# Kernel tuning notes

Measured on AMD Instinct MI355X. Metric: run time of the kernel, lower is better.

Reference implementation:

```python
import jax, jax.numpy as jnp
import numpy as np

B, S, D, H = 2, 2048, 1024, 16
DK = D // H


def layernorm(x, gamma, bias, eps=1e-6):
    m = jnp.mean(x, axis=-1, keepdims=True)
    v = jnp.mean((x - m) ** 2, axis=-1, keepdims=True)  # biased var (correction=0)
    return gamma * (x - m) / jnp.sqrt(v + eps) + bias


def setup_inputs() -> dict:
    key = jax.random.key(0)
    ks = jax.random.split(key, 10)
    xav = (2.0 / (D + D)) ** 0.5  # xavier_normal_ std for square [D,D]
    lin1_b = (1.0 / D) ** 0.5     # nn.Linear default init bound
    lin2_b = (1.0 / (4 * D)) ** 0.5
    return {
        "X": jax.random.normal(ks[0], (B, S, D), jnp.float32),
        "padding_mask": jnp.ones((B, 1, S), jnp.int32),
        "W_Q": jax.random.normal(ks[1], (D, D), jnp.float32) * xav,
        "W_K": jax.random.normal(ks[2], (D, D), jnp.float32) * xav,
        "W_V": jax.random.normal(ks[3], (D, D), jnp.float32) * xav,
        "W_O": jax.random.normal(ks[4], (D, D), jnp.float32) * xav,
        "g1": jnp.ones((D,), jnp.float32),
        "b1": jnp.zeros((D,), jnp.float32),
        "W1": jax.random.uniform(ks[5], (D, 4 * D), jnp.float32, -lin1_b, lin1_b),
        "bias1": jax.random.uniform(ks[6], (4 * D,), jnp.float32, -lin1_b, lin1_b),
        "W2": jax.random.uniform(ks[7], (4 * D, D), jnp.float32, -lin2_b, lin2_b),
        "bias2": jax.random.uniform(ks[8], (D,), jnp.float32, -lin2_b, lin2_b),
        "g2": jnp.ones((D,), jnp.float32),
        "b2": jnp.zeros((D,), jnp.float32),
    }


def reference(X, padding_mask, W_Q, W_K, W_V, W_O, g1, b1, W1, bias1, W2, bias2, g2, b2):
    b, s, d = X.shape
    # pre-norm + MHA
    xn = layernorm(X, g1, b1)
    q = (xn @ W_Q).reshape(b, s, H, DK).transpose(0, 2, 1, 3)  # [B,H,S,DK]
    k = (xn @ W_K).reshape(b, s, H, DK).transpose(0, 2, 1, 3)
    v = (xn @ W_V).reshape(b, s, H, DK).transpose(0, 2, 1, 3)
    scores = jnp.einsum("bhqd,bhkd->bhqk", q, k) / np.sqrt(DK).astype(np.float32)
    mask = padding_mask[:, None, :, :]  # [B,1,1,S] broadcast over heads/queries
    scores = jnp.where(mask == 0, jnp.float32(-1e9), scores)
    w = jax.nn.softmax(scores, axis=-1)
    attn = jnp.einsum("bhqk,bhkd->bhqd", w, v)
    attn = attn.transpose(0, 2, 1, 3).reshape(b, s, d) @ W_O
    out = attn + X
    # pre-norm + GELU FFN (exact erf GELU, matching nn.GELU default)
    nn2 = layernorm(out, g2, b2)
    ff = jax.nn.gelu(nn2 @ W1 + bias1, approximate=False) @ W2 + bias2
    return ff + out
```

## Files before the change

kernel.cpp:

```cpp
#include <hip/hip_runtime.h>
#include <hip/hip_bf16.h>


using bf16 = __hip_bfloat16;
typedef __attribute__((ext_vector_type(4))) float f32x4;
typedef __attribute__((ext_vector_type(16))) float f32x16;
typedef __attribute__((ext_vector_type(8))) short bf16x8;

#define DEVI static __device__ __forceinline__

DEVI void async_copy16(const void* g, void* l) {
  __builtin_amdgcn_global_load_lds(
      (const __attribute__((address_space(1))) void*)g,
      (__attribute__((address_space(3))) void*)l, 16, 0, 0);
}

DEVI ushort f2bf_bits(float v) {
  __hip_bfloat16 h = __float2bfloat16(v);
  return *reinterpret_cast<ushort*>(&h);
}

DEVI float bfbits2f(ushort u) {
  union { float f; unsigned int i; } x;
  x.i = ((unsigned int)u) << 16;
  return x.f;
}

DEVI unsigned int pk2(float lo, float hi) {
  return (unsigned int)f2bf_bits(lo) | ((unsigned int)f2bf_bits(hi) << 16);
}

__global__ __launch_bounds__(256) void ln_kernel(
    const float* __restrict__ in, const float* __restrict__ gamma,
    const float* __restrict__ beta, bf16* __restrict__ out) {
  const long row = blockIdx.x;
  const int t = threadIdx.x;
  float4 x = ((const float4*)(in + row * 1024))[t];
  float s = x.x + x.y + x.z + x.w;
  float s2 = x.x * x.x + x.y * x.y + x.z * x.z + x.w * x.w;
#pragma unroll
  for (int m = 1; m < 64; m <<= 1) {
    s += __shfl_xor(s, m);
    s2 += __shfl_xor(s2, m);
  }
  __shared__ float red[8];
  const int w = t >> 6, l = t & 63;
  if (l == 0) { red[w] = s; red[4 + w] = s2; }
  __syncthreads();
  s = red[0] + red[1] + red[2] + red[3];
  s2 = red[4] + red[5] + red[6] + red[7];
  const float mean = s * (1.0f / 1024.0f);
  const float var = s2 * (1.0f / 1024.0f) - mean * mean;
  const float rstd = rsqrtf(var + 1e-6f);
  float4 g4 = ((const float4*)gamma)[t];
  float4 b4 = ((const float4*)beta)[t];
  union { ushort h[4]; uint2 u; } o;
  o.h[0] = f2bf_bits(g4.x * (x.x - mean) * rstd + b4.x);
  o.h[1] = f2bf_bits(g4.y * (x.y - mean) * rstd + b4.y);
  o.h[2] = f2bf_bits(g4.z * (x.z - mean) * rstd + b4.z);
  o.h[3] = f2bf_bits(g4.w * (x.w - mean) * rstd + b4.w);
  ((uint2*)(out + row * 1024))[t] = o.u;
}

__global__ __launch_bounds__(256) void oproj_reduce_ln(
    const float* __restrict__ p0, const float* __restrict__ p1,
    const float* __restrict__ X, const float* __restrict__ gamma,
    const float* __restrict__ beta, float* __restrict__ res_out,
    bf16* __restrict__ xn_out) {
  const long row = blockIdx.x;
  const int t = threadIdx.x;
  const long i = row * 256 + t;
  const float4 a = ((const float4*)p0)[i];
  const float4 b = ((const float4*)p1)[i];
  const float4 c = ((const float4*)X)[i];
  float4 x;
  x.x = a.x + b.x + c.x; x.y = a.y + b.y + c.y;
  x.z = a.z + b.z + c.z; x.w = a.w + b.w + c.w;
  ((float4*)res_out)[i] = x;
  float s = x.x + x.y + x.z + x.w;
  float s2 = x.x * x.x + x.y * x.y + x.z * x.z + x.w * x.w;
#pragma unroll
  for (int m = 1; m < 64; m <<= 1) {
    s += __shfl_xor(s, m);
    s2 += __shfl_xor(s2, m);
  }
  __shared__ float red[8];
  const int w = t >> 6, l = t & 63;
  if (l == 0) { red[w] = s; red[4 + w] = s2; }
  __syncthreads();
  s = red[0] + red[1] + red[2] + red[3];
  s2 = red[4] + red[5] + red[6] + red[7];
  const float mean = s * (1.0f / 1024.0f);
  const float var = s2 * (1.0f / 1024.0f) - mean * mean;
  const float rstd = rsqrtf(var + 1e-6f);
  float4 g4 = ((const float4*)gamma)[t];
  float4 b4 = ((const float4*)beta)[t];
  union { ushort h[4]; uint2 u; } o;
  o.h[0] = f2bf_bits(g4.x * (x.x - mean) * rstd + b4.x);
  o.h[1] = f2bf_bits(g4.y * (x.y - mean) * rstd + b4.y);
  o.h[2] = f2bf_bits(g4.z * (x.z - mean) * rstd + b4.z);
  o.h[3] = f2bf_bits(g4.w * (x.w - mean) * rstd + b4.w);
  ((uint2*)(xn_out + row * 1024))[t] = o.u;
}

__global__ __launch_bounds__(256) void transpose_all(
    const float* __restrict__ q, const float* __restrict__ k,
    const float* __restrict__ v, const float* __restrict__ o,
    const float* __restrict__ w1, const float* __restrict__ w2,
    bf16* __restrict__ wqkvo, bf16* __restrict__ w1t, bf16* __restrict__ w2t) {
  const int tid = blockIdx.x;
  const float* W;
  bf16* Wt;
  int K, N, n0, k0;
  if (tid < 4096) {
    const int z = tid >> 10, r = tid & 1023;
    W = (z == 0) ? q : (z == 1) ? k : (z == 2) ? v : o;
    Wt = wqkvo + (size_t)z * 1024 * 1024;
    K = 1024; N = 1024; n0 = (r & 31) << 5; k0 = (r >> 5) << 5;
  } else if (tid < 8192) {
    const int r = tid - 4096;
    W = w1; Wt = w1t; K = 1024; N = 4096;
    n0 = (r & 127) << 5; k0 = (r >> 7) << 5;
  } else {
    const int r = tid - 8192;
    W = w2; Wt = w2t; K = 4096; N = 1024;
    n0 = (r & 31) << 5; k0 = (r >> 5) << 5;
  }
  __shared__ float tile[32][33];
  const int tx = threadIdx.x & 31, ty = threadIdx.x >> 5;
#pragma unroll
  for (int i = 0; i < 32; i += 8)
    tile[ty + i][tx] = W[(long)(k0 + ty + i) * N + n0 + tx];
  __syncthreads();
#pragma unroll
  for (int i = 0; i < 32; i += 8)
    Wt[(long)(n0 + ty + i) * K + k0 + tx] = __float2bfloat16(tile[tx][ty + i]);
}

template <int EPI, int KSPLIT>
__global__ __launch_bounds__(256) void gemm_bt(
    const bf16* __restrict__ A, const bf16* __restrict__ Bt,
    const int M, const int N, const int K, const int lda, const int ldb,
    const float* __restrict__ bias, const float* __restrict__ res,
    float* __restrict__ pother, void* __restrict__ Cout) {
  __shared__ __align__(16) char gsmem[65536];
  const int t = threadIdx.x;
  const int w = t >> 6, l = t & 63;
  const int nb = N >> 7;
  const int cpx = gridDim.x >> 3;
  int bidx = (blockIdx.x & 7) * cpx + (blockIdx.x >> 3);
  int sl = 0;
  if (KSPLIT == 2) {
    const int half = gridDim.x >> 1;
    sl = bidx >= half;
    bidx -= sl * half;
  }
  const int bm = bidx / nb, bn = bidx % nb;
  const long row0 = (long)bm << 7, col0 = (long)bn << 7;
  const int wr = (w >> 1) << 6, wc = (w & 1) << 6;
  const int lr = l & 15;
  const int lkb = (l >> 4) << 4;

  f32x4 acc[4][4];
#pragma unroll
  for (int m = 0; m < 4; ++m)
#pragma unroll
    for (int n = 0; n < 4; ++n) acc[m][n] = (f32x4){0.f, 0.f, 0.f, 0.f};

  const int rA = t >> 3;
  const int g = (t & 7) ^ ((t >> 3) & 7);
  const bf16* gA = A + (row0 + rA) * (long)lda + (long)sl * K + g * 8;
  const bf16* gB = Bt + (col0 + rA) * (long)ldb + (long)sl * K + g * 8;

  const int nt = K >> 6;
#pragma unroll
  for (int cr = 0; cr < 4; ++cr) {
    async_copy16(gA + (long)cr * 32 * lda, gsmem + t * 16 + cr * 4096);
    async_copy16(gB + (long)cr * 32 * ldb, gsmem + 16384 + t * 16 + cr * 4096);
  }
  int cur = 0;

  for (int kt = 0; kt < nt; ++kt) {
    if (kt < nt - 1) {
      const int k1 = (kt + 1) << 6;
      char* dst = gsmem + (cur ^ 1) * 32768;
#pragma unroll
      for (int cr = 0; cr < 4; ++cr) {
        async_copy16(gA + (long)cr * 32 * lda + k1, dst + t * 16 + cr * 4096);
        async_copy16(gB + (long)cr * 32 * ldb + k1, dst + 16384 + t * 16 + cr * 4096);
      }
      asm volatile("s_waitcnt vmcnt(8)" ::: "memory");
    } else {
      asm volatile("s_waitcnt vmcnt(0)" ::: "memory");
    }
    __builtin_amdgcn_s_barrier();
    __builtin_amdgcn_sched_barrier(0);
    const char* As = gsmem + cur * 32768;
    const char* Bs = As + 16384;
#pragma unroll
    for (int ks = 0; ks < 2; ++ks) {
      bf16x8 af[4], bfr[4];
#pragma unroll
      for (int m = 0; m < 4; ++m) {
        const int row = wr + m * 16 + lr;
        af[m] = *(const bf16x8*)(As +
            (row * 128 + ((ks * 64 + lkb) ^ ((row & 7) << 4))));
      }
#pragma unroll
      for (int n = 0; n < 4; ++n) {
        const int row = wc + n * 16 + lr;
        bfr[n] = *(const bf16x8*)(Bs +
            (row * 128 + ((ks * 64 + lkb) ^ ((row & 7) << 4))));
      }
#pragma unroll
      for (int m = 0; m < 4; ++m)
#pragma unroll
        for (int n = 0; n < 4; ++n)
          acc[m][n] = __builtin_amdgcn_mfma_f32_16x16x32_bf16(af[m], bfr[n], acc[m][n], 0, 0, 0);
    }
    __builtin_amdgcn_sched_barrier(0);
    __builtin_amdgcn_s_barrier();
    cur ^= 1;
  }

  bf16* Cb = (bf16*)Cout;
  float* Cf = (float*)Cout;
  if ((EPI == 4 || EPI == 5) && sl == 1) Cf = pother;
#pragma unroll
  for (int m = 0; m < 4; ++m) {
#pragma unroll
    for (int r = 0; r < 4; ++r) {
      const long crow = row0 + wr + m * 16 + ((l >> 4) << 2) + r;
      const long rbase = crow * N;
#pragma unroll
      for (int n = 0; n < 4; ++n) {
        const long ccol = col0 + wc + n * 16 + lr;
        float v = acc[m][n][r];
        if (EPI == 2) {
          const float vv = v + bias[ccol];
          const float u2 = vv * (1.5957691216f + 0.0713548162f * vv * vv);
          v = vv / (1.0f + __expf(-u2));
        }
        if (EPI == 5 && sl == 0) v += bias[ccol] + res[rbase + ccol];
        if (EPI == 0 || EPI == 2)
          Cb[rbase + ccol] = __float2bfloat16(v);
        else
          Cf[rbase + ccol] = v;
      }
    }
  }
}

__global__ __launch_bounds__(256) void ff2_reduce(
    const float* __restrict__ p0, const float* __restrict__ p1,
    float* __restrict__ out) {
  const int idx = blockIdx.x * 256 + threadIdx.x;
  const float4 x = ((const float4*)p0)[idx];
  const float4 y = ((const float4*)p1)[idx];
  float4 a;
  a.x = x.x + y.x; a.y = x.y + y.y; a.z = x.z + y.z; a.w = x.w + y.w;
  ((float4*)out)[idx] = a;
}

__global__ __launch_bounds__(512) void attn_kernel(
    const bf16* __restrict__ QKV, const int* __restrict__ pmask,
    bf16* __restrict__ Oout) {
  const int bh = blockIdx.x;
  const int b = bh >> 4, h = bh & 15;
  const int q0 = blockIdx.y << 8;
  const int t = threadIdx.x;
  const int w = t >> 6, l = t & 63;
  const int lq = l & 31, hi = l >> 5;

  __shared__ __align__(16) char smem[65536];

  const long base = (long)b * 2048 * 3072;
  const bf16* Qg = QKV + base + h * 64;
  const bf16* Kg = QKV + base + 1024 + h * 64;
  const bf16* Vg = QKV + base + 2048 + h * 64;

  int kSrc[2], kDst[2], vk[2], vsg[2];
#pragma unroll
  for (int p = 0; p < 2; ++p) {
    const int c = p * 512 + t;
    const int kr = c >> 3;
    kSrc[p] = kr * 3072 + (((c & 7) ^ (kr & 7)) << 3);
    kDst[p] = c * 16;
    vk[p] = c >> 3;
    vsg[p] = c & 7;
  }

  const int qw0 = q0 + w * 32;
  bf16x8 qf[4];
#pragma unroll
  for (int dc = 0; dc < 4; ++dc) {
    uint4 raw = *(const uint4*)(Qg + (long)(qw0 + lq) * 3072 + dc * 16 + hi * 8);
    union { uint4 u4; ushort us[8]; } in; in.u4 = raw;
    union { bf16x8 v; ushort us[8]; } o;
#pragma unroll
    for (int e = 0; e < 8; ++e) o.us[e] = f2bf_bits(0.125f * bfbits2f(in.us[e]));
    qf[dc] = o.v;
  }

  union { unsigned int u[4]; bf16x8 v; } bones;
  bones.u[0] = (hi == 0) ? 0x00003F80u : 0u;
  bones.u[1] = bones.u[2] = bones.u[3] = 0u;

  uint4 vreg[2];
#pragma unroll
  for (int p = 0; p < 2; ++p) {
    vreg[p] = *(const uint4*)(Vg + (long)vk[p] * 3072 + vsg[p] * 8);
    async_copy16(Kg + kSrc[p], smem + kDst[p]);
  }
#pragma unroll
  for (int p = 0; p < 2; ++p) {
    const ushort* vs = (const ushort*)&vreg[p];
#pragma unroll
    for (int e = 0; e < 8; ++e) {
      const int d = vsg[p] * 8 + e;
      *(ushort*)(smem + 32768 + d * 256 +
                 ((vk[p] * 2) ^ (((e ^ vsg[p]) & 7) << 4))) = vs[e];
    }
  }

  f32x16 oacc[2];
#pragma unroll
  for (int nt = 0; nt < 2; ++nt)
#pragma unroll
    for (int r = 0; r < 16; ++r) oacc[nt][r] = 0.f;
  float mrun = -3.0e38f, lsum = 0.f;
  int cur = 0;

  __syncthreads();

  for (int ktg = 0; ktg < 16; ++ktg) {
    if (ktg < 15) {
      const long nrow0 = (long)(ktg + 1) * 128 * 3072;
#pragma unroll
      for (int p = 0; p < 2; ++p) {
        vreg[p] = *(const uint4*)(Vg + nrow0 + (long)vk[p] * 3072 + vsg[p] * 8);
        async_copy16(Kg + nrow0 + kSrc[p], smem + (cur ^ 1) * 16384 + kDst[p]);
      }
    }
    const int k0 = ktg << 7;
    const char* Ks = smem + cur * 16384;
    const char* Vt = smem + 32768 + cur * 16384;

    f32x16 sacc[4];
    __builtin_amdgcn_s_setprio(1);
#pragma unroll
    for (int kt = 0; kt < 4; ++kt) {
#pragma unroll
      for (int r = 0; r < 16; ++r) sacc[kt][r] = 0.f;
#pragma unroll
      for (int dc = 0; dc < 4; ++dc) {
        bf16x8 ka = *(const bf16x8*)(Ks +
            ((kt * 32 + lq) * 128 + ((dc * 32 + hi * 16) ^ ((lq & 7) << 4))));
        sacc[kt] = __builtin_amdgcn_mfma_f32_32x32x16_bf16(ka, qf[dc], sacc[kt], 0, 0, 0);
      }
      const int mv = pmask[b * 2048 + k0 + kt * 32 + lq];
      union { unsigned int u[4]; bf16x8 v; } aadd;
      aadd.u[0] = (hi == 0 && mv == 0) ? (unsigned int)f2bf_bits(-1.0e9f) : 0u;
      aadd.u[1] = aadd.u[2] = aadd.u[3] = 0u;
      sacc[kt] = __builtin_amdgcn_mfma_f32_32x32x16_bf16(aadd.v, bones.v, sacc[kt], 0, 0, 0);
    }
    __builtin_amdgcn_s_setprio(0);

    float tmax = -3.0e38f;
#pragma unroll
    for (int kt = 0; kt < 4; ++kt)
#pragma unroll
      for (int r = 0; r < 16; ++r) tmax = fmaxf(tmax, sacc[kt][r]);
    tmax = fmaxf(tmax, __shfl_xor(tmax, 32));
    const bool need = (bool)__any(tmax > mrun + 8.0f);
    const float mnew = need ? fmaxf(mrun, tmax) : mrun;
    float psum = 0.f;
#pragma unroll
    for (int kt = 0; kt < 4; ++kt)
#pragma unroll
      for (int r = 0; r < 16; ++r) {
        const float p = __expf(sacc[kt][r] - mnew);
        sacc[kt][r] = p;
        psum += p;
      }
    psum += __shfl_xor(psum, 32);
    if (need) {
      const float alpha = __expf(mrun - mnew);
      mrun = mnew;
      lsum = lsum * alpha + psum;
#pragma unroll
      for (int r = 0; r < 16; ++r) {
        const float ar = __shfl(alpha, (r & 3) + 8 * (r >> 2) + 4 * hi);
        oacc[0][r] *= ar;
        oacc[1][r] *= ar;
      }
    } else {
      lsum += psum;
    }

    union { unsigned int u[4]; bf16x8 v; } paE[4], paO[4];
#pragma unroll
    for (int kt = 0; kt < 4; ++kt) {
      const unsigned int cs0 = pk2(sacc[kt][0], sacc[kt][1]);
      const unsigned int cs1 = pk2(sacc[kt][2], sacc[kt][3]);
      const unsigned int cs2 = pk2(sacc[kt][4], sacc[kt][5]);
      const unsigned int cs3 = pk2(sacc[kt][6], sacc[kt][7]);
      const unsigned int cs4 = pk2(sacc[kt][8], sacc[kt][9]);
      const unsigned int cs5 = pk2(sacc[kt][10], sacc[kt][11]);
      const unsigned int cs6 = pk2(sacc[kt][12], sacc[kt][13]);
      const unsigned int cs7 = pk2(sacc[kt][14], sacc[kt][15]);
      const unsigned int es0 = __shfl_xor(cs0, 32);
      const unsigned int es1 = __shfl_xor(cs1, 32);
      const unsigned int es2 = __shfl_xor(cs2, 32);
      const unsigned int es3 = __shfl_xor(cs3, 32);
      const unsigned int es4 = __shfl_xor(cs4, 32);
      const unsigned int es5 = __shfl_xor(cs5, 32);
      const unsigned int es6 = __shfl_xor(cs6, 32);
      const unsigned int es7 = __shfl_xor(cs7, 32);
      paE[kt].u[0] = hi ? es2 : cs0;
      paE[kt].u[1] = hi ? es3 : cs1;
      paE[kt].u[2] = hi ? cs2 : es0;
      paE[kt].u[3] = hi ? cs3 : es1;
      paO[kt].u[0] = hi ? es6 : cs4;
      paO[kt].u[1] = hi ? es7 : cs5;
      paO[kt].u[2] = hi ? cs6 : es4;
      paO[kt].u[3] = hi ? cs7 : es5;
    }

    __builtin_amdgcn_s_setprio(1);
#pragma unroll
    for (int kt = 0; kt < 4; ++kt)
#pragma unroll
      for (int nt = 0; nt < 2; ++nt) {
        const int vrow = nt * 32 + lq;
        const int vsw = ((vrow & 7) ^ ((vrow >> 3) & 7)) << 4;
        bf16x8 vbE = *(const bf16x8*)(Vt + (vrow * 256 + ((kt * 64 + hi * 16) ^ vsw)));
        oacc[nt] = __builtin_amdgcn_mfma_f32_32x32x16_bf16(paE[kt].v, vbE, oacc[nt], 0, 0, 0);
        bf16x8 vbO = *(const bf16x8*)(Vt + (vrow * 256 + ((kt * 64 + 32 + hi * 16) ^ vsw)));
        oacc[nt] = __builtin_amdgcn_mfma_f32_32x32x16_bf16(paO[kt].v, vbO, oacc[nt], 0, 0, 0);
      }
    __builtin_amdgcn_s_setprio(0);

    if (ktg < 15) {
      char* VtN = smem + 32768 + (cur ^ 1) * 16384;
#pragma unroll
      for (int p = 0; p < 2; ++p) {
        const ushort* vs = (const ushort*)&vreg[p];
#pragma unroll
        for (int e = 0; e < 8; ++e) {
          const int d = vsg[p] * 8 + e;
          *(ushort*)(VtN + d * 256 +
                     ((vk[p] * 2) ^ (((e ^ vsg[p]) & 7) << 4))) = vs[e];
        }
      }
    }

    __syncthreads();
    cur ^= 1;
  }

  const float inv = 1.0f / lsum;
#pragma unroll
  for (int r = 0; r < 16; ++r) {
    const int crow = (r & 3) + 8 * (r >> 2) + 4 * hi;
    const float ir = __shfl(inv, crow);
    const long orow = (long)b * 2048 + qw0 + crow;
#pragma unroll
    for (int nt = 0; nt < 2; ++nt)
      Oout[orow * 1024 + h * 64 + nt * 32 + lq] = __float2bfloat16(oacc[nt][r] * ir);
  }
}

extern "C" void kernel_launch(void* const* d_in, const int* in_sizes, int n_in,
                              void* d_out, int out_size, void* d_ws, size_t ws_size,
                              hipStream_t stream) {
  const float* X = (const float*)d_in[0];
  const int* pmask = (const int*)d_in[1];
  const float* W_Q = (const float*)d_in[2];
  const float* W_K = (const float*)d_in[3];
  const float* W_V = (const float*)d_in[4];
  const float* W_O = (const float*)d_in[5];
  const float* g1 = (const float*)d_in[6];
  const float* b1 = (const float*)d_in[7];
  const float* W1 = (const float*)d_in[8];
  const float* bias1 = (const float*)d_in[9];
  const float* W2 = (const float*)d_in[10];
  const float* bias2 = (const float*)d_in[11];
  const float* g2 = (const float*)d_in[12];
  const float* b2 = (const float*)d_in[13];
  (void)in_sizes; (void)n_in; (void)out_size; (void)ws_size;

  char* ws = (char*)d_ws;
  const size_t MB = 1ull << 20;
  bf16* W1_t   = (bf16*)(ws + 0);
  bf16* Wqkv_t = (bf16*)(ws + 8 * MB);
  bf16* Wo_t   = (bf16*)(ws + 14 * MB);
  bf16* W2_t   = (bf16*)(ws + 16 * MB);
  bf16* xn     = (bf16*)(ws + 24 * MB);
  bf16* QKV    = (bf16*)(ws + 32 * MB);
  bf16* attnb  = (bf16*)(ws + 56 * MB);
  bf16* ff1    = (bf16*)(ws + 32 * MB);
  float* p0o   = (float*)(ws + 64 * MB);
  float* p1o   = (float*)(ws + 32 * MB);
  float* p0    = (float*)(ws + 64 * MB);
  float* p1    = (float*)(ws + 0);
  float* res1  = (float*)d_out;

  transpose_all<<<12288, 256, 0, stream>>>(W_Q, W_K, W_V, W_O, W1, W2,
                                           Wqkv_t, W1_t, W2_t);
  ln_kernel<<<4096, 256, 0, stream>>>(X, g1, b1, xn);
  gemm_bt<0, 1><<<32 * 24, 256, 0, stream>>>(xn, Wqkv_t, 4096, 3072, 1024, 1024, 1024,
                                             nullptr, nullptr, nullptr, QKV);
  attn_kernel<<<dim3(32, 8), 512, 0, stream>>>(QKV, pmask, attnb);
  gemm_bt<4, 2><<<2 * 32 * 8, 256, 0, stream>>>(attnb, Wo_t, 4096, 1024, 512, 1024, 1024,
                                                nullptr, nullptr, p1o, p0o);
  oproj_reduce_ln<<<4096, 256, 0, stream>>>(p0o, p1o, X, g2, b2, res1, xn);
  gemm_bt<2, 1><<<32 * 32, 256, 0, stream>>>(xn, W1_t, 4096, 4096, 1024, 1024, 1024,
                                             bias1, nullptr, nullptr, ff1);
  gemm_bt<5, 2><<<2 * 32 * 8, 256, 0, stream>>>(ff1, W2_t, 4096, 1024, 2048, 4096, 4096,
                                                bias2, res1, p1, p0);
  ff2_reduce<<<4096, 256, 0, stream>>>(p0, p1, res1);
}
```

Baseline: 267.6 us.

## Triple-buffer GEMM A tiles with deeper prefetch and fuse LN1 into transpose

The GEMM now keeps three LDS buffers for the A tile and two for B. A is prefetched two k-steps ahead and B one step ahead, with the vmcnt waits adjusted to match. This is meant to hide more global-load latency in the main loop, but raises LDS use from 64KB to 80KB per block, which may cut occupancy. Separately, the first layernorm is folded into the weight-transpose kernel as extra blocks, removing one kernel launch.

```diff
diff --git a/kernel.cpp b/kernel.cpp
--- a/kernel.cpp
+++ b/kernel.cpp
@@ -30,36 +30,70 @@
   return (unsigned int)f2bf_bits(lo) | ((unsigned int)f2bf_bits(hi) << 16);
 }
 
-__global__ __launch_bounds__(256) void ln_kernel(
-    const float* __restrict__ in, const float* __restrict__ gamma,
-    const float* __restrict__ beta, bf16* __restrict__ out) {
-  const long row = blockIdx.x;
-  const int t = threadIdx.x;
-  float4 x = ((const float4*)(in + row * 1024))[t];
-  float s = x.x + x.y + x.z + x.w;
-  float s2 = x.x * x.x + x.y * x.y + x.z * x.z + x.w * x.w;
-#pragma unroll
-  for (int m = 1; m < 64; m <<= 1) {
-    s += __shfl_xor(s, m);
-    s2 += __shfl_xor(s2, m);
-  }
-  __shared__ float red[8];
-  const int w = t >> 6, l = t & 63;
-  if (l == 0) { red[w] = s; red[4 + w] = s2; }
+__global__ __launch_bounds__(256) void transpose_all_ln(
+    const float* __restrict__ q, const float* __restrict__ k,
+    const float* __restrict__ v, const float* __restrict__ o,
+    const float* __restrict__ w1, const float* __restrict__ w2,
+    bf16* __restrict__ wqkvo, bf16* __restrict__ w1t, bf16* __restrict__ w2t,
+    const float* __restrict__ X, const float* __restrict__ g1,
+    const float* __restrict__ b1, bf16* __restrict__ xn) {
+  const int tid = blockIdx.x;
+  if (tid >= 12288) {
+    const long row = tid - 12288;
+    const int t = threadIdx.x;
+    float4 x = ((const float4*)(X + row * 1024))[t];
+    float s = x.x + x.y + x.z + x.w;
+    float s2 = x.x * x.x + x.y * x.y + x.z * x.z + x.w * x.w;
+#pragma unroll
+    for (int m = 1; m < 64; m <<= 1) {
+      s += __shfl_xor(s, m);
+      s2 += __shfl_xor(s2, m);
+    }
+    __shared__ float red[8];
+    const int w = t >> 6, l = t & 63;
+    if (l == 0) { red[w] = s; red[4 + w] = s2; }
+    __syncthreads();
+    s = red[0] + red[1] + red[2] + red[3];
+    s2 = red[4] + red[5] + red[6] + red[7];
+    const float mean = s * (1.0f / 1024.0f);
+    const float var = s2 * (1.0f / 1024.0f) - mean * mean;
+    const float rstd = rsqrtf(var + 1e-6f);
+    float4 g4 = ((const float4*)g1)[t];
+    float4 b4 = ((const float4*)b1)[t];
+    union { ushort h[4]; uint2 u; } oo;
+    oo.h[0] = f2bf_bits(g4.x * (x.x - mean) * rstd + b4.x);
+    oo.h[1] = f2bf_bits(g4.y * (x.y - mean) * rstd + b4.y);
+    oo.h[2] = f2bf_bits(g4.z * (x.z - mean) * rstd + b4.z);
+    oo.h[3] = f2bf_bits(g4.w * (x.w - mean) * rstd + b4.w);
+    ((uint2*)(xn + row * 1024))[t] = oo.u;
+    return;
+  }
+  const float* W;
+  bf16* Wt;
+  int K, N, n0, k0;
+  if (tid < 4096) {
+    const int z = tid >> 10, r = tid & 1023;
+    W = (z == 0) ? q : (z == 1) ? k : (z == 2) ? v : o;
+    Wt = wqkvo + (size_t)z * 1024 * 1024;
+    K = 1024; N = 1024; n0 = (r & 31) << 5; k0 = (r >> 5) << 5;
+  } else if (tid < 8192) {
+    const int r = tid - 4096;
+    W = w1; Wt = w1t; K = 1024; N = 4096;
+    n0 = (r & 127) << 5; k0 = (r >> 7) << 5;
+  } else {
+    const int r = tid - 8192;
+    W = w2; Wt = w2t; K = 4096; N = 1024;
+    n0 = (r & 31) << 5; k0 = (r >> 5) << 5;
+  }
+  __shared__ float tile[32][33];
+  const int tx = threadIdx.x & 31, ty = threadIdx.x >> 5;
+#pragma unroll
+  for (int i = 0; i < 32; i += 8)
+    tile[ty + i][tx] = W[(long)(k0 + ty + i) * N + n0 + tx];
   __syncthreads();
-  s = red[0] + red[1] + red[2] + red[3];
-  s2 = red[4] + red[5] + red[6] + red[7];
-  const float mean = s * (1.0f / 1024.0f);
-  const float var = s2 * (1.0f / 1024.0f) - mean * mean;
-  const float rstd = rsqrtf(var + 1e-6f);
-  float4 g4 = ((const float4*)gamma)[t];
-  float4 b4 = ((const float4*)beta)[t];
-  union { ushort h[4]; uint2 u; } o;
-  o.h[0] = f2bf_bits(g4.x * (x.x - mean) * rstd + b4.x);
-  o.h[1] = f2bf_bits(g4.y * (x.y - mean) * rstd + b4.y);
-  o.h[2] = f2bf_bits(g4.z * (x.z - mean) * rstd + b4.z);
-  o.h[3] = f2bf_bits(g4.w * (x.w - mean) * rstd + b4.w);
-  ((uint2*)(out + row * 1024))[t] = o.u;
+#pragma unroll
+  for (int i = 0; i < 32; i += 8)
+    Wt[(long)(n0 + ty + i) * K + k0 + tx] = __float2bfloat16(tile[tx][ty + i]);
 }
 
 __global__ __launch_bounds__(256) void oproj_reduce_ln(
@@ -103,47 +137,13 @@
   ((uint2*)(xn_out + row * 1024))[t] = o.u;
 }
 
-__global__ __launch_bounds__(256) void transpose_all(
-    const float* __restrict__ q, const float* __restrict__ k,
-    const float* __restrict__ v, const float* __restrict__ o,
-    const float* __restrict__ w1, const float* __restrict__ w2,
-    bf16* __restrict__ wqkvo, bf16* __restrict__ w1t, bf16* __restrict__ w2t) {
-  const int tid = blockIdx.x;
-  const float* W;
-  bf16* Wt;
-  int K, N, n0, k0;
-  if (tid < 4096) {
-    const int z = tid >> 10, r = tid & 1023;
-    W = (z == 0) ? q : (z == 1) ? k : (z == 2) ? v : o;
-    Wt = wqkvo + (size_t)z * 1024 * 1024;
-    K = 1024; N = 1024; n0 = (r & 31) << 5; k0 = (r >> 5) << 5;
-  } else if (tid < 8192) {
-    const int r = tid - 4096;
-    W = w1; Wt = w1t; K = 1024; N = 4096;
-    n0 = (r & 127) << 5; k0 = (r >> 7) << 5;
-  } else {
-    const int r = tid - 8192;
-    W = w2; Wt = w2t; K = 4096; N = 1024;
-    n0 = (r & 31) << 5; k0 = (r >> 5) << 5;
-  }
-  __shared__ float tile[32][33];
-  const int tx = threadIdx.x & 31, ty = threadIdx.x >> 5;
-#pragma unroll
-  for (int i = 0; i < 32; i += 8)
-    tile[ty + i][tx] = W[(long)(k0 + ty + i) * N + n0 + tx];
-  __syncthreads();
-#pragma unroll
-  for (int i = 0; i < 32; i += 8)
-    Wt[(long)(n0 + ty + i) * K + k0 + tx] = __float2bfloat16(tile[tx][ty + i]);
-}
-
 template <int EPI, int KSPLIT>
 __global__ __launch_bounds__(256) void gemm_bt(
     const bf16* __restrict__ A, const bf16* __restrict__ Bt,
     const int M, const int N, const int K, const int lda, const int ldb,
     const float* __restrict__ bias, const float* __restrict__ res,
     float* __restrict__ pother, void* __restrict__ Cout) {
-  __shared__ __align__(16) char gsmem[65536];
+  __shared__ __align__(16) char gsmem[81920];
   const int t = threadIdx.x;
   const int w = t >> 6, l = t & 63;
   const int nb = N >> 7;
@@ -171,32 +171,46 @@
   const int g = (t & 7) ^ ((t >> 3) & 7);
   const bf16* gA = A + (row0 + rA) * (long)lda + (long)sl * K + g * 8;
   const bf16* gB = Bt + (col0 + rA) * (long)ldb + (long)sl * K + g * 8;
+  char* const Bbase = gsmem + 49152;
 
   const int nt = K >> 6;
 #pragma unroll
-  for (int cr = 0; cr < 4; ++cr) {
+  for (int cr = 0; cr < 4; ++cr)
     async_copy16(gA + (long)cr * 32 * lda, gsmem + t * 16 + cr * 4096);
-    async_copy16(gB + (long)cr * 32 * ldb, gsmem + 16384 + t * 16 + cr * 4096);
-  }
-  int cur = 0;
+#pragma unroll
+  for (int cr = 0; cr < 4; ++cr)
+    async_copy16(gB + (long)cr * 32 * ldb, Bbase + t * 16 + cr * 4096);
+#pragma unroll
+  for (int cr = 0; cr < 4; ++cr)
+    async_copy16(gA + (long)cr * 32 * lda + 64, gsmem + 16384 + t * 16 + cr * 4096);
+  int curB = 0;
 
   for (int kt = 0; kt < nt; ++kt) {
-    if (kt < nt - 1) {
+    if (kt + 1 < nt) {
       const int k1 = (kt + 1) << 6;
-      char* dst = gsmem + (cur ^ 1) * 32768;
-#pragma unroll
-      for (int cr = 0; cr < 4; ++cr) {
-        async_copy16(gA + (long)cr * 32 * lda + k1, dst + t * 16 + cr * 4096);
-        async_copy16(gB + (long)cr * 32 * ldb + k1, dst + 16384 + t * 16 + cr * 4096);
-      }
+      char* dstB = Bbase + (curB ^ 1) * 16384;
+#pragma unroll
+      for (int cr = 0; cr < 4; ++cr)
+        async_copy16(gB + (long)cr * 32 * ldb + k1, dstB + t * 16 + cr * 4096);
+    }
+    if (kt + 2 < nt) {
+      const int k2 = (kt + 2) << 6;
+      char* dstA = gsmem + ((kt + 2) % 3) * 16384;
+#pragma unroll
+      for (int cr = 0; cr < 4; ++cr)
+        async_copy16(gA + (long)cr * 32 * lda + k2, dstA + t * 16 + cr * 4096);
+    }
+    if (kt < nt - 2) {
+      asm volatile("s_waitcnt vmcnt(12)" ::: "memory");
+    } else if (kt == nt - 2) {
       asm volatile("s_waitcnt vmcnt(8)" ::: "memory");
     } else {
       asm volatile("s_waitcnt vmcnt(0)" ::: "memory");
     }
     __builtin_amdgcn_s_barrier();
     __builtin_amdgcn_sched_barrier(0);
-    const char* As = gsmem + cur * 32768;
-    const char* Bs = As + 16384;
+    const char* As = gsmem + (kt % 3) * 16384;
+    const char* Bs = Bbase + curB * 16384;
 #pragma unroll
     for (int ks = 0; ks < 2; ++ks) {
       bf16x8 af[4], bfr[4];
@@ -220,7 +234,7 @@
     }
     __builtin_amdgcn_sched_barrier(0);
     __builtin_amdgcn_s_barrier();
-    cur ^= 1;
+    curB ^= 1;
   }
 
   bf16* Cb = (bf16*)Cout;
@@ -506,9 +520,9 @@
   float* p1    = (float*)(ws + 0);
   float* res1  = (float*)d_out;
 
-  transpose_all<<<12288, 256, 0, stream>>>(W_Q, W_K, W_V, W_O, W1, W2,
-                                           Wqkv_t, W1_t, W2_t);
-  ln_kernel<<<4096, 256, 0, stream>>>(X, g1, b1, xn);
+  transpose_all_ln<<<16384, 256, 0, stream>>>(W_Q, W_K, W_V, W_O, W1, W2,
+                                              Wqkv_t, W1_t, W2_t,
+                                              X, g1, b1, xn);
   gemm_bt<0, 1><<<32 * 24, 256, 0, stream>>>(xn, Wqkv_t, 4096, 3072, 1024, 1024, 1024,
                                              nullptr, nullptr, nullptr, QKV);
   attn_kernel<<<dim3(32, 8), 512, 0, stream>>>(QKV, pmask, attnb);
```

New measurement: 264.1 us. About the same (-1.3%).
